# Kernel tuning notes

Hardware: AMD Instinct MI355X
Metric: run time of the kernel (lower is better)

The kernel has to match this reference:

```python
import jax, jax.numpy as jnp
import numpy as np

DIM = 768
HEADS = 8
DHEAD = 64
DEMB = HEADS * DHEAD  # 512
EPS = 1e-5


def layer_norm(x, g, b):
    mu = jnp.mean(x, axis=-1, keepdims=True)
    var = jnp.var(x, axis=-1, keepdims=True)
    return (x - mu) * jax.lax.rsqrt(var + EPS) * g + b


def setup_inputs() -> dict:
    key = jax.random.key(0)
    ks = jax.random.split(key, 9)
    b, t, n_src, n_ltn = 2, 4, 8192, 64
    inv = 1.0 / np.sqrt(DIM)
    return {
        "src": jax.random.normal(ks[0], (b, t, n_src, DIM), jnp.float32),
        "ltn": jax.random.normal(ks[1], (b, t, n_ltn, DIM), jnp.float32),
        "g_src": jnp.ones((DIM,), jnp.float32),
        "b_src": jnp.zeros((DIM,), jnp.float32),
        "g_ltn": jnp.ones((DIM,), jnp.float32),
        "b_ltn": jnp.zeros((DIM,), jnp.float32),
        # weights stored (in, out) so y = x @ W  (== torch Linear with W.T)
        "Wq": jax.random.normal(ks[2], (DIM, DEMB), jnp.float32) * inv,
        "Wkv": jax.random.normal(ks[3], (DIM, 2 * DEMB), jnp.float32) * inv,
        "Wo": jax.random.normal(ks[4], (DEMB, DIM), jnp.float32) * (1.0 / np.sqrt(DEMB)),
    }


def reference(src, ltn, g_src, b_src, g_ltn, b_ltn, Wq, Wkv, Wo):
    b, t, n_ltn, _ = ltn.shape
    n_src = src.shape[2]
    scale = DHEAD ** -0.5

    src_n = layer_norm(src, g_src, b_src)
    ltn_n = layer_norm(ltn, g_ltn, b_ltn)

    q = ltn_n @ Wq                                  # [b,t,nl,DEMB]
    ctx = jnp.concatenate([src_n, ltn_n], axis=-2)  # [b,t,ns+nl,DIM]
    kv = ctx @ Wkv                                  # [b,t,ns+nl,2*DEMB]
    k, v = jnp.split(kv, 2, axis=-1)

    def to_heads(x):  # b t n (h d) -> b h t n d
        B, T, N, _ = x.shape
        return x.reshape(B, T, N, HEADS, DHEAD).transpose(0, 3, 1, 2, 4)

    q, k, v = to_heads(q), to_heads(k), to_heads(v)

    attn = jnp.einsum('bhtid,bhtjd->bhtij', q, k) * scale
    attn = jax.nn.softmax(attn - jax.lax.stop_gradient(attn.max(axis=-1, keepdims=True)), axis=-1)
    out = jnp.einsum('bhtij,bhtjd->bhtid', attn, v)  # [b,h,t,nl,d]

    out = out.transpose(0, 2, 3, 1, 4).reshape(b, t, n_ltn, DEMB)
    return out @ Wo
```

## Files before the change

### kernel.cpp

```cpp
#include <hip/hip_runtime.h>
#include <hip/hip_bf16.h>
#include <type_traits>


#define N_SRC 8192
#define N_LTN 64
#define N_CTX 8256
#define NBT 8
#define MROWS 66048
#define DIMK 768
#define DEMB 512
#define NSPLIT 16
#define NTILES 65

typedef short short8 __attribute__((ext_vector_type(8)));
typedef float floatx4 __attribute__((ext_vector_type(4)));
typedef __attribute__((address_space(1))) void gvoid;
typedef __attribute__((address_space(3))) void lvoid;

__device__ inline ushort f2bf(float f) {
    union { float f; unsigned u; } v; v.f = f;
    unsigned u = v.u;
    return (ushort)((u + 0x7fffu + ((u >> 16) & 1u)) >> 16);
}

__global__ __launch_bounds__(256) void transpose_bf16(
        const float* __restrict__ in, ushort* __restrict__ out, int R, int C) {
    int gid = blockIdx.x * 256 + threadIdx.x;
    if (gid >= R * C) return;
    int c = gid / R, r = gid - c * R;
    out[gid] = f2bf(in[(size_t)r * C + c]);
}

__global__ __launch_bounds__(256) void ln_kernel(
        const float* __restrict__ src, const float* __restrict__ ltn,
        const float* __restrict__ gs, const float* __restrict__ bs,
        const float* __restrict__ gl, const float* __restrict__ bl,
        ushort* __restrict__ ctx, ushort* __restrict__ qin) {
    int r = blockIdx.x * 4 + (threadIdx.x >> 6);
    int lane = threadIdx.x & 63;
    int bt = r / N_CTX;
    int i = r - bt * N_CTX;
    const float *x, *g, *b;
    int isl = (i >= N_SRC);
    if (!isl) { x = src + ((size_t)bt * N_SRC + i) * DIMK; g = gs; b = bs; }
    else      { x = ltn + ((size_t)bt * N_LTN + (i - N_SRC)) * DIMK; g = gl; b = bl; }
    float v[12]; float s = 0.f, s2 = 0.f;
#pragma unroll
    for (int t = 0; t < 12; t++) {
        float xv = x[lane + t * 64];
        v[t] = xv; s += xv; s2 += xv * xv;
    }
#pragma unroll
    for (int off = 32; off >= 1; off >>= 1) {
        s  += __shfl_xor(s,  off, 64);
        s2 += __shfl_xor(s2, off, 64);
    }
    float mu  = s * (1.0f / 768.0f);
    float var = s2 * (1.0f / 768.0f) - mu * mu;
    float rs  = rsqrtf(var + 1e-5f);
    ushort* crow = ctx + (size_t)r * DIMK;
    ushort* qrow = isl ? (qin + (size_t)(bt * N_LTN + (i - N_SRC)) * DIMK) : nullptr;
#pragma unroll
    for (int t = 0; t < 12; t++) {
        int idx = lane + t * 64;
        float y = (v[t] - mu) * rs * g[idx] + b[idx];
        ushort hb = f2bf(y);
        crow[idx] = hb;
        if (isl) qrow[idx] = hb;
    }
}

template <typename CT>
__global__ __launch_bounds__(256) void gemm_bt(
        const ushort* __restrict__ A, const ushort* __restrict__ B,
        CT* __restrict__ C, int M, int N, int K) {
    __shared__ ushort lA[128 * 64];
    __shared__ ushort lB[128 * 64];
    int tid = threadIdx.x;
    int lane = tid & 63, wave = tid >> 6;
    int wm = wave >> 1, wn = wave & 1;
    int bm = blockIdx.x, bn = blockIdx.y;

    floatx4 acc[4][4];
#pragma unroll
    for (int mi = 0; mi < 4; mi++)
#pragma unroll
        for (int ni = 0; ni < 4; ni++) acc[mi][ni] = (floatx4){0.f, 0.f, 0.f, 0.f};

    int srow = lane >> 3;
    int schunk = (lane & 7) ^ srow;
    int quad = lane >> 4, lr = lane & 15;
    const int kiters = K >> 6;

    for (int kt = 0; kt < kiters; kt++) {
#pragma unroll
        for (int c2 = 0; c2 < 4; c2++) {
            int row = c2 * 32 + wave * 8 + srow;
            const ushort* gpA = A + ((size_t)(bm * 128 + row) * K + kt * 64 + schunk * 8);
            ushort* lpA = lA + (c2 * 32 + wave * 8) * 64 + lane * 8;
            __builtin_amdgcn_global_load_lds((gvoid*)gpA, (lvoid*)lpA, 16, 0, 0);
            const ushort* gpB = B + ((size_t)(bn * 128 + row) * K + kt * 64 + schunk * 8);
            ushort* lpB = lB + (c2 * 32 + wave * 8) * 64 + lane * 8;
            __builtin_amdgcn_global_load_lds((gvoid*)gpB, (lvoid*)lpB, 16, 0, 0);
        }
        __syncthreads();
#pragma unroll
        for (int ks = 0; ks < 2; ks++) {
            short8 av[4], bv[4];
            int slot = ((ks * 4 + quad) ^ (lane & 7)) * 8;
#pragma unroll
            for (int mi = 0; mi < 4; mi++)
                av[mi] = *(const short8*)(lA + (wm * 64 + mi * 16 + lr) * 64 + slot);
#pragma unroll
            for (int ni = 0; ni < 4; ni++)
                bv[ni] = *(const short8*)(lB + (wn * 64 + ni * 16 + lr) * 64 + slot);
#pragma unroll
            for (int mi = 0; mi < 4; mi++)
#pragma unroll
                for (int ni = 0; ni < 4; ni++)
                    acc[mi][ni] = __builtin_amdgcn_mfma_f32_16x16x32_bf16(
                        av[mi], bv[ni], acc[mi][ni], 0, 0, 0);
        }
        __syncthreads();
    }
#pragma unroll
    for (int mi = 0; mi < 4; mi++)
#pragma unroll
        for (int ni = 0; ni < 4; ni++)
#pragma unroll
            for (int r = 0; r < 4; r++) {
                int row = bm * 128 + wm * 64 + mi * 16 + quad * 4 + r;
                int col = bn * 128 + wn * 64 + ni * 16 + lr;
                float vv = acc[mi][ni][r];
                if constexpr (std::is_same<CT, ushort>::value)
                    C[(size_t)row * N + col] = f2bf(vv);
                else
                    C[(size_t)row * N + col] = vv;
            }
}

#define PR 136

__global__ __launch_bounds__(256) void attn_flash(
        const float* __restrict__ qf, const ushort* __restrict__ kvb,
        float* __restrict__ Op, float* __restrict__ ml) {
    __shared__ ushort lK[128 * 64];
    __shared__ ushort lVT[64 * PR];
    __shared__ ushort lP[64 * PR];
    __shared__ float smax[64 * 4];
    __shared__ float psum[64 * 4];
    __shared__ float mnew[64];
    __shared__ float salpha[64];

    int comb = blockIdx.x, split = blockIdx.y;
    int bt = comb >> 3, h = comb & 7;
    int tid = threadIdx.x;
    int w = tid >> 6, lane = tid & 63, quad = lane >> 4, lr = lane & 15;

    const ushort* kptr = kvb + (size_t)bt * N_CTX * 1024 + h * 64;
    const ushort* vptr = kptr + 512;

    short8 qa[4][2];
    {
        const float* qbase = qf + (size_t)(bt * 64) * DEMB + h * 64;
#pragma unroll
        for (int mi = 0; mi < 4; mi++)
#pragma unroll
            for (int kc = 0; kc < 2; kc++) {
                const float* p = qbase + (size_t)(mi * 16 + lr) * DEMB + kc * 32 + quad * 8;
                float4 f0 = *(const float4*)p;
                float4 f1 = *(const float4*)(p + 4);
                short8 v;
                v[0] = f2bf(f0.x); v[1] = f2bf(f0.y); v[2] = f2bf(f0.z); v[3] = f2bf(f0.w);
                v[4] = f2bf(f1.x); v[5] = f2bf(f1.y); v[6] = f2bf(f1.z); v[7] = f2bf(f1.w);
                qa[mi][kc] = v;
            }
    }

    floatx4 accO[4];
#pragma unroll
    for (int nt = 0; nt < 4; nt++) accO[nt] = (floatx4){0.f, 0.f, 0.f, 0.f};
    float m_run = -1e30f, l_run = 0.f;

    int vp = tid & 63;
    int vdg = tid >> 6;

    for (int t = split; t < NTILES; t += NSPLIT) {
        int kbase = t * 128;
        __syncthreads();

#pragma unroll
        for (int c2 = 0; c2 < 4; c2++) {
            int jloc = w * 32 + c2 * 8 + (lane >> 3);
            int chunk = (lane & 7) ^ ((lane >> 3) & 7);
            const ushort* gp = kptr + (size_t)(kbase + jloc) * 1024 + chunk * 8;
            ushort* lp = lK + (w * 32 + c2 * 8) * 64 + lane * 8;
            __builtin_amdgcn_global_load_lds((gvoid*)gp, (lvoid*)lp, 16, 0, 0);
        }

        {
            int k0 = kbase + vp * 2;
            bool valid = (k0 + 1) < N_CTX;
            const ushort* r0 = vptr + (size_t)k0 * 1024 + vdg * 16;
            const ushort* r1 = r0 + 1024;
            uint4 a0 = *(const uint4*)r0;
            uint4 a1 = *(const uint4*)(r0 + 8);
            uint4 b0 = *(const uint4*)r1;
            uint4 b1 = *(const uint4*)(r1 + 8);
            if (!valid) {
                a0 = make_uint4(0, 0, 0, 0); a1 = a0; b0 = a0; b1 = a0;
            }
            unsigned av8[8] = {a0.x, a0.y, a0.z, a0.w, a1.x, a1.y, a1.z, a1.w};
            unsigned bv8[8] = {b0.x, b0.y, b0.z, b0.w, b1.x, b1.y, b1.z, b1.w};
#pragma unroll
            for (int i = 0; i < 8; i++) {
                unsigned la = av8[i] & 0xffffu, ha = av8[i] >> 16;
                unsigned lb = bv8[i] & 0xffffu, hb = bv8[i] >> 16;
                *(unsigned*)(lVT + (vdg * 16 + 2 * i) * PR + vp * 2)     = la | (lb << 16);
                *(unsigned*)(lVT + (vdg * 16 + 2 * i + 1) * PR + vp * 2) = ha | (hb << 16);
            }
        }
        __syncthreads();

        floatx4 accS[4][2];
#pragma unroll
        for (int mi = 0; mi < 4; mi++)
#pragma unroll
            for (int nt = 0; nt < 2; nt++) accS[mi][nt] = (floatx4){0.f, 0.f, 0.f, 0.f};
#pragma unroll
        for (int kc = 0; kc < 2; kc++) {
            short8 bv[2];
#pragma unroll
            for (int nt = 0; nt < 2; nt++) {
                int kr = w * 32 + nt * 16 + lr;
                int slot = (kc * 4 + quad) ^ (kr & 7);
                bv[nt] = *(const short8*)(lK + kr * 64 + slot * 8);
            }
#pragma unroll
            for (int mi = 0; mi < 4; mi++)
#pragma unroll
                for (int nt = 0; nt < 2; nt++)
                    accS[mi][nt] = __builtin_amdgcn_mfma_f32_16x16x32_bf16(
                        qa[mi][kc], bv[nt], accS[mi][nt], 0, 0, 0);
        }

        bool v0 = (kbase + w * 32 + lr) < N_CTX;
        bool v1 = (kbase + w * 32 + 16 + lr) < N_CTX;
        float sc[4][2][4];
#pragma unroll
        for (int mi = 0; mi < 4; mi++)
#pragma unroll
            for (int r = 0; r < 4; r++) {
                sc[mi][0][r] = v0 ? accS[mi][0][r] * 0.125f : -1e30f;
                sc[mi][1][r] = v1 ? accS[mi][1][r] * 0.125f : -1e30f;
            }
#pragma unroll
        for (int mi = 0; mi < 4; mi++)
#pragma unroll
            for (int r = 0; r < 4; r++) {
                float m = fmaxf(sc[mi][0][r], sc[mi][1][r]);
#pragma unroll
                for (int d = 1; d < 16; d <<= 1) m = fmaxf(m, __shfl_xor(m, d, 64));
                if (lr == 0) smax[(mi * 16 + quad * 4 + r) * 4 + w] = m;
            }
        __syncthreads();

        if (w == 0) {
            float4 s4 = *(const float4*)(smax + lane * 4);
            float mt = fmaxf(fmaxf(s4.x, s4.y), fmaxf(s4.z, s4.w));
            float mn = fmaxf(m_run, mt);
            salpha[lane] = __expf(m_run - mn);
            m_run = mn;
            mnew[lane] = mn;
        }
        __syncthreads();

#pragma unroll
        for (int mi = 0; mi < 4; mi++)
#pragma unroll
            for (int r = 0; r < 4; r++) {
                int row = mi * 16 + quad * 4 + r;
                float mrow = mnew[row];
                float p0 = __expf(sc[mi][0][r] - mrow);
                float p1 = __expf(sc[mi][1][r] - mrow);
                lP[row * PR + w * 32 + lr]      = f2bf(p0);
                lP[row * PR + w * 32 + 16 + lr] = f2bf(p1);
                float s = p0 + p1;
#pragma unroll
                for (int d = 1; d < 16; d <<= 1) s += __shfl_xor(s, d, 64);
                if (lr == 0) psum[row * 4 + w] = s;
            }
        {
            float a0 = salpha[w * 16 + quad * 4 + 0];
            float a1 = salpha[w * 16 + quad * 4 + 1];
            float a2 = salpha[w * 16 + quad * 4 + 2];
            float a3 = salpha[w * 16 + quad * 4 + 3];
#pragma unroll
            for (int nt = 0; nt < 4; nt++) {
                accO[nt][0] *= a0; accO[nt][1] *= a1;
                accO[nt][2] *= a2; accO[nt][3] *= a3;
            }
        }
        __syncthreads();

        if (w == 0) {
            float4 p4 = *(const float4*)(psum + lane * 4);
            l_run = l_run * salpha[lane] + (p4.x + p4.y + p4.z + p4.w);
        }

        short8 av[4];
#pragma unroll
        for (int kc = 0; kc < 4; kc++)
            av[kc] = *(const short8*)(lP + (w * 16 + lr) * PR + kc * 32 + quad * 8);
#pragma unroll
        for (int nt = 0; nt < 4; nt++)
#pragma unroll
            for (int kc = 0; kc < 4; kc++) {
                short8 bv = *(const short8*)(lVT + (nt * 16 + lr) * PR + kc * 32 + quad * 8);
                accO[nt] = __builtin_amdgcn_mfma_f32_16x16x32_bf16(av[kc], bv, accO[nt], 0, 0, 0);
            }
    }

    float* opb = Op + (size_t)(comb * NSPLIT + split) * 64 * 64;
#pragma unroll
    for (int nt = 0; nt < 4; nt++)
#pragma unroll
        for (int r = 0; r < 4; r++)
            opb[(w * 16 + quad * 4 + r) * 64 + nt * 16 + lr] = accO[nt][r];
    if (w == 0) {
        float* mlp = ml + ((size_t)(comb * NSPLIT + split) * 64 + lane) * 2;
        mlp[0] = m_run; mlp[1] = l_run;
    }
}

__global__ __launch_bounds__(64) void attn_combine(
        const float* __restrict__ Op, const float* __restrict__ ml,
        ushort* __restrict__ outp) {
    int bx = blockIdx.x;
    int comb = bx >> 6, q = bx & 63;
    int bt = comb >> 3, h = comb & 7;
    int d = threadIdx.x;
    float mv[NSPLIT], lv[NSPLIT];
    float M = -1e30f;
#pragma unroll
    for (int s = 0; s < NSPLIT; s++) {
        const float* p = ml + ((size_t)(comb * NSPLIT + s) * 64 + q) * 2;
        mv[s] = p[0]; lv[s] = p[1];
        M = fmaxf(M, mv[s]);
    }
    float L = 0.f, O = 0.f;
#pragma unroll
    for (int s = 0; s < NSPLIT; s++) {
        float wgt = __expf(mv[s] - M);
        L += wgt * lv[s];
        O += wgt * Op[((size_t)(comb * NSPLIT + s) * 64 + q) * 64 + d];
    }
    outp[(size_t)(bt * 64 + q) * DEMB + h * 64 + d] = f2bf(O / L);
}

extern "C" void kernel_launch(void* const* d_in, const int* in_sizes, int n_in,
                              void* d_out, int out_size, void* d_ws, size_t ws_size,
                              hipStream_t stream) {
    const float* src   = (const float*)d_in[0];
    const float* ltn   = (const float*)d_in[1];
    const float* g_src = (const float*)d_in[2];
    const float* b_src = (const float*)d_in[3];
    const float* g_ltn = (const float*)d_in[4];
    const float* b_ltn = (const float*)d_in[5];
    const float* Wq    = (const float*)d_in[6];
    const float* Wkv   = (const float*)d_in[7];
    const float* Wo    = (const float*)d_in[8];
    float* out = (float*)d_out;

    char* ws = (char*)d_ws;
    size_t off = 0;
    auto alloc = [&](size_t bytes) -> void* {
        void* p = ws + off;
        off += (bytes + 255) & ~(size_t)255;
        return p;
    };
    ushort* ctx  = (ushort*)alloc((size_t)MROWS * DIMK * 2);
    ushort* qin  = (ushort*)alloc((size_t)512 * DIMK * 2);
    ushort* WkvT = (ushort*)alloc((size_t)1024 * DIMK * 2);
    ushort* WqT  = (ushort*)alloc((size_t)512 * DIMK * 2);
    ushort* WoT  = (ushort*)alloc((size_t)768 * DEMB * 2);
    ushort* kvb  = (ushort*)alloc((size_t)MROWS * 1024 * 2);
    float*  qf   = (float*) alloc((size_t)512 * DEMB * 4);
    ushort* outp = (ushort*)alloc((size_t)512 * DEMB * 2);

    float* Op  = (float*)(void*)ctx;
    float* mlb = Op + (size_t)64 * NSPLIT * 64 * 64;

    transpose_bf16<<<(768 * 1024 + 255) / 256, 256, 0, stream>>>(Wkv, WkvT, 768, 1024);
    transpose_bf16<<<(768 * 512 + 255) / 256, 256, 0, stream>>>(Wq, WqT, 768, 512);
    transpose_bf16<<<(512 * 768 + 255) / 256, 256, 0, stream>>>(Wo, WoT, 512, 768);

    ln_kernel<<<MROWS / 4, 256, 0, stream>>>(src, ltn, g_src, b_src, g_ltn, b_ltn, ctx, qin);

    gemm_bt<ushort><<<dim3(MROWS / 128, 1024 / 128), 256, 0, stream>>>(
        ctx, WkvT, kvb, MROWS, 1024, DIMK);
    gemm_bt<float><<<dim3(512 / 128, 512 / 128), 256, 0, stream>>>(
        qin, WqT, qf, 512, 512, DIMK);

    attn_flash<<<dim3(64, NSPLIT), 256, 0, stream>>>(qf, kvb, Op, mlb);
    attn_combine<<<4096, 64, 0, stream>>>(Op, mlb, outp);

    gemm_bt<float><<<dim3(512 / 128, 768 / 128), 256, 0, stream>>>(
        outp, WoT, out, 512, 768, DEMB);
}
```

Baseline: 583.4 us.

## Tile weight transposes, vectorize layernorm, swap GEMM grid order, double attention splits

Merges the three per-element weight transposes into one LDS-tiled kernel with coalesced reads and writes. Vectorizes the layernorm loads and stores to float4/ushort4. Swaps the GEMM block index mapping so consecutive blocks share the same A row tile for better L2 reuse. Raises the attention split count from 16 to 32 for more parallelism, clamps out-of-range K/V addresses, and makes the combine kernel loop without per-split arrays; this adds more partial outputs and combine work.

```diff
diff --git a/kernel.cpp b/kernel.cpp
--- a/kernel.cpp
+++ b/kernel.cpp
@@ -10,7 +10,7 @@
 #define MROWS 66048
 #define DIMK 768
 #define DEMB 512
-#define NSPLIT 16
+#define NSPLIT 32
 #define NTILES 65
 
 typedef short short8 __attribute__((ext_vector_type(8)));
@@ -24,12 +24,30 @@
     return (ushort)((u + 0x7fffu + ((u >> 16) & 1u)) >> 16);
 }
 
-__global__ __launch_bounds__(256) void transpose_bf16(
-        const float* __restrict__ in, ushort* __restrict__ out, int R, int C) {
-    int gid = blockIdx.x * 256 + threadIdx.x;
-    if (gid >= R * C) return;
-    int c = gid / R, r = gid - c * R;
-    out[gid] = f2bf(in[(size_t)r * C + c]);
+__global__ __launch_bounds__(256) void transpose_all(
+        const float* __restrict__ Wkv, const float* __restrict__ Wq,
+        const float* __restrict__ Wo, ushort* __restrict__ WkvT,
+        ushort* __restrict__ WqT, ushort* __restrict__ WoT) {
+    __shared__ ushort tile[64][65];
+    int z = blockIdx.z;
+    const float* in; ushort* out; int R, C;
+    if (z == 0)      { in = Wkv; out = WkvT; R = 768; C = 1024; }
+    else if (z == 1) { in = Wq;  out = WqT;  R = 768; C = 512;  }
+    else             { in = Wo;  out = WoT;  R = 512; C = 768;  }
+    int C0 = blockIdx.x * 64, R0 = blockIdx.y * 64;
+    if (C0 >= C || R0 >= R) return;
+    int tc = threadIdx.x & 63, tr4 = threadIdx.x >> 6;
+#pragma unroll
+    for (int j = 0; j < 16; j++) {
+        int r = tr4 + j * 4;
+        tile[r][tc] = f2bf(in[(size_t)(R0 + r) * C + C0 + tc]);
+    }
+    __syncthreads();
+#pragma unroll
+    for (int j = 0; j < 16; j++) {
+        int c = tr4 + j * 4;
+        out[(size_t)(C0 + c) * R + R0 + tc] = tile[tc][c];
+    }
 }
 
 __global__ __launch_bounds__(256) void ln_kernel(
@@ -45,11 +63,13 @@
     int isl = (i >= N_SRC);
     if (!isl) { x = src + ((size_t)bt * N_SRC + i) * DIMK; g = gs; b = bs; }
     else      { x = ltn + ((size_t)bt * N_LTN + (i - N_SRC)) * DIMK; g = gl; b = bl; }
-    float v[12]; float s = 0.f, s2 = 0.f;
-#pragma unroll
-    for (int t = 0; t < 12; t++) {
-        float xv = x[lane + t * 64];
-        v[t] = xv; s += xv; s2 += xv * xv;
+    float4 v[3]; float s = 0.f, s2 = 0.f;
+#pragma unroll
+    for (int t = 0; t < 3; t++) {
+        float4 xv = *(const float4*)(x + t * 256 + lane * 4);
+        v[t] = xv;
+        s  += xv.x + xv.y + xv.z + xv.w;
+        s2 += xv.x * xv.x + xv.y * xv.y + xv.z * xv.z + xv.w * xv.w;
     }
 #pragma unroll
     for (int off = 32; off >= 1; off >>= 1) {
@@ -62,12 +82,17 @@
     ushort* crow = ctx + (size_t)r * DIMK;
     ushort* qrow = isl ? (qin + (size_t)(bt * N_LTN + (i - N_SRC)) * DIMK) : nullptr;
 #pragma unroll
-    for (int t = 0; t < 12; t++) {
-        int idx = lane + t * 64;
-        float y = (v[t] - mu) * rs * g[idx] + b[idx];
-        ushort hb = f2bf(y);
-        crow[idx] = hb;
-        if (isl) qrow[idx] = hb;
+    for (int t = 0; t < 3; t++) {
+        int idx = t * 256 + lane * 4;
+        float4 gv = *(const float4*)(g + idx);
+        float4 bv = *(const float4*)(b + idx);
+        ushort4 u;
+        u.x = f2bf((v[t].x - mu) * rs * gv.x + bv.x);
+        u.y = f2bf((v[t].y - mu) * rs * gv.y + bv.y);
+        u.z = f2bf((v[t].z - mu) * rs * gv.z + bv.z);
+        u.w = f2bf((v[t].w - mu) * rs * gv.w + bv.w);
+        *(ushort4*)(crow + idx) = u;
+        if (isl) *(ushort4*)(qrow + idx) = u;
     }
 }
 
@@ -80,7 +105,7 @@
     int tid = threadIdx.x;
     int lane = tid & 63, wave = tid >> 6;
     int wm = wave >> 1, wn = wave & 1;
-    int bm = blockIdx.x, bn = blockIdx.y;
+    int bn = blockIdx.x, bm = blockIdx.y;
 
     floatx4 acc[4][4];
 #pragma unroll
@@ -194,7 +219,8 @@
         for (int c2 = 0; c2 < 4; c2++) {
             int jloc = w * 32 + c2 * 8 + (lane >> 3);
             int chunk = (lane & 7) ^ ((lane >> 3) & 7);
-            const ushort* gp = kptr + (size_t)(kbase + jloc) * 1024 + chunk * 8;
+            int jg = kbase + jloc; if (jg > N_CTX - 1) jg = N_CTX - 1;
+            const ushort* gp = kptr + (size_t)jg * 1024 + chunk * 8;
             ushort* lp = lK + (w * 32 + c2 * 8) * 64 + lane * 8;
             __builtin_amdgcn_global_load_lds((gvoid*)gp, (lvoid*)lp, 16, 0, 0);
         }
@@ -202,7 +228,8 @@
         {
             int k0 = kbase + vp * 2;
             bool valid = (k0 + 1) < N_CTX;
-            const ushort* r0 = vptr + (size_t)k0 * 1024 + vdg * 16;
+            int k0c = valid ? k0 : (N_CTX - 2);
+            const ushort* r0 = vptr + (size_t)k0c * 1024 + vdg * 16;
             const ushort* r1 = r0 + 1024;
             uint4 a0 = *(const uint4*)r0;
             uint4 a1 = *(const uint4*)(r0 + 8);
@@ -341,20 +368,15 @@
     int comb = bx >> 6, q = bx & 63;
     int bt = comb >> 3, h = comb & 7;
     int d = threadIdx.x;
-    float mv[NSPLIT], lv[NSPLIT];
     float M = -1e30f;
-#pragma unroll
+    for (int s = 0; s < NSPLIT; s++)
+        M = fmaxf(M, ml[((size_t)(comb * NSPLIT + s) * 64 + q) * 2]);
+    float L = 0.f, O = 0.f;
     for (int s = 0; s < NSPLIT; s++) {
         const float* p = ml + ((size_t)(comb * NSPLIT + s) * 64 + q) * 2;
-        mv[s] = p[0]; lv[s] = p[1];
-        M = fmaxf(M, mv[s]);
-    }
-    float L = 0.f, O = 0.f;
-#pragma unroll
-    for (int s = 0; s < NSPLIT; s++) {
-        float wgt = __expf(mv[s] - M);
-        L += wgt * lv[s];
-        O += wgt * Op[((size_t)(comb * NSPLIT + s) * 64 + q) * 64 + d];
+        float wgt = __expf(p[0] - M);
+        L = fmaf(wgt, p[1], L);
+        O = fmaf(wgt, Op[((size_t)(comb * NSPLIT + s) * 64 + q) * 64 + d], O);
     }
     outp[(size_t)(bt * 64 + q) * DEMB + h * 64 + d] = f2bf(O / L);
 }
@@ -392,13 +414,11 @@
     float* Op  = (float*)(void*)ctx;
     float* mlb = Op + (size_t)64 * NSPLIT * 64 * 64;
 
-    transpose_bf16<<<(768 * 1024 + 255) / 256, 256, 0, stream>>>(Wkv, WkvT, 768, 1024);
-    transpose_bf16<<<(768 * 512 + 255) / 256, 256, 0, stream>>>(Wq, WqT, 768, 512);
-    transpose_bf16<<<(512 * 768 + 255) / 256, 256, 0, stream>>>(Wo, WoT, 512, 768);
+    transpose_all<<<dim3(16, 12, 3), 256, 0, stream>>>(Wkv, Wq, Wo, WkvT, WqT, WoT);
 
     ln_kernel<<<MROWS / 4, 256, 0, stream>>>(src, ltn, g_src, b_src, g_ltn, b_ltn, ctx, qin);
 
-    gemm_bt<ushort><<<dim3(MROWS / 128, 1024 / 128), 256, 0, stream>>>(
+    gemm_bt<ushort><<<dim3(1024 / 128, MROWS / 128), 256, 0, stream>>>(
         ctx, WkvT, kvb, MROWS, 1024, DIMK);
     gemm_bt<float><<<dim3(512 / 128, 512 / 128), 256, 0, stream>>>(
         qin, WqT, qf, 512, 512, DIMK);
@@ -406,6 +426,6 @@
     attn_flash<<<dim3(64, NSPLIT), 256, 0, stream>>>(qf, kvb, Op, mlb);
     attn_combine<<<4096, 64, 0, stream>>>(Op, mlb, outp);
 
-    gemm_bt<float><<<dim3(512 / 128, 768 / 128), 256, 0, stream>>>(
+    gemm_bt<float><<<dim3(768 / 128, 512 / 128), 256, 0, stream>>>(
         outp, WoT, out, 512, 768, DEMB);
 }
```

Measured after the change: 568.5 us. -2.6%, faster.
